# Performance work log

Measured on AMD Instinct MI355X. Metric: run time of the kernel, lower is better.

## Reference

```python
import jax, jax.numpy as jnp
import numpy as np

BLKQ = 64
BLKK = 64
TOPK_RATIO = 0.25
EPS = 1e-05


def mean_pool(x, blk):
    B, H, L, D = x.shape
    return x.reshape(B, H, L // blk, blk, D).mean(axis=3)


def setup_inputs() -> dict:
    key = jax.random.key(0)
    kq, kk, kv, kw, kb = jax.random.split(key, 5)
    B, H, Lq, Lk, D = 1, 8, 4096, 4096, 64
    q = jax.random.normal(kq, (B, H, Lq, D), dtype=jnp.float32)
    k = jax.random.normal(kk, (B, H, Lk, D), dtype=jnp.float32)
    v = jax.random.normal(kv, (B, H, Lk, D), dtype=jnp.float32)
    # proj_l is zero-initialized in the original; use small random weights so the
    # linear-attention branch contributes non-trivially to the output.
    proj_w = jax.random.normal(kw, (D, D), dtype=jnp.float32) * 0.02
    proj_b = jax.random.normal(kb, (D,), dtype=jnp.float32) * 0.02
    return {"q": q, "k": k, "v": v, "proj_w": proj_w, "proj_b": proj_b}


def reference(q, k, v, proj_w, proj_b):
    B, H, Lq, D = q.shape
    Lk = k.shape[2]
    nQ, nK = Lq // BLKQ, Lk // BLKK

    # ---- block-level top-k routing (get_block_map_cross) ----
    arg_k = k - k.mean(axis=-2, keepdims=True)
    pq = mean_pool(q, BLKQ)                      # (B,H,nQ,D)
    pk = mean_pool(arg_k, BLKK)                  # (B,H,nK,D)
    pooled_score = jnp.einsum('bhqd,bhkd->bhqk', pq, pk)  # (B,H,nQ,nK)
    topk = min(nK, max(1, int(TOPK_RATIO * nK)))
    lut = jax.lax.top_k(pooled_score, topk)[1]   # (B,H,nQ,topk) int32

    # ---- block-sparse cross attention (softmax over selected K blocks) ----
    qb = q.reshape(B, H, nQ, BLKQ, D)
    kb = k.reshape(B, H, nK, BLKK, D)
    vb = v.reshape(B, H, nK, BLKK, D)
    gather = jax.vmap(jax.vmap(lambda blocks, idx: blocks[idx]))  # over B,H
    kg = gather(kb, lut)                         # (B,H,nQ,topk,BLKK,D)
    vg = gather(vb, lut)                         # (B,H,nQ,topk,BLKK,D)
    scale = D ** -0.5
    s = jnp.einsum('bhnqd,bhntkd->bhnqtk', qb, kg) * scale
    s = s.reshape(B, H, nQ, BLKQ, topk * BLKK)
    p = jax.nn.softmax(s, axis=-1)
    o_s = jnp.einsum('bhnqt,bhntd->bhnqd', p, vg.reshape(B, H, nQ, topk * BLKK, D))
    o_s = o_s.reshape(B, H, Lq, D)

    # ---- linear attention branch (softmax feature map, tied q/k) ----
    qf = jax.nn.softmax(q, axis=-1)
    kf = jax.nn.softmax(k, axis=-1)
    kv = jnp.einsum('bhkd,bhke->bhde', kf, v)    # (B,H,D,D)
    denom = jnp.einsum('bhqd,bhd->bhq', qf, kf.sum(axis=2)) + EPS
    o_l = jnp.einsum('bhqd,bhde->bhqe', qf, kv) / denom[..., None]
    o_l = o_l @ proj_w.T + proj_b                # proj_l

    return o_s + o_l
```

## Files before the change

kernel.cpp:

```cpp
#include <hip/hip_runtime.h>
#include <math.h>

#define H 8
#define L 4096
#define D 64
#define NBLK 64
#define TOPK 16
#define EPS 1e-5f
#define LP 68

typedef unsigned short u16;
typedef unsigned int u32;
typedef __attribute__((ext_vector_type(8))) short bf16x8;
typedef __attribute__((ext_vector_type(16))) float f32x16;
typedef __attribute__((ext_vector_type(4))) u32 u32x4;

static __device__ __forceinline__ u16 f2bf(float x) {
  u32 u = __float_as_uint(x);
  u32 r = (u + 0x7fffu + ((u >> 16) & 1u)) >> 16;
  return (u16)r;
}
static __device__ __forceinline__ float bf2f(u16 h) {
  return __uint_as_float(((u32)h) << 16);
}
__device__ __forceinline__ float dot4f(float4 a, float4 b) {
  return a.x * b.x + a.y * b.y + a.z * b.z + a.w * b.w;
}
static __device__ __forceinline__ void async_cp16(uint4* lds, const uint4* g) {
  __builtin_amdgcn_global_load_lds(
      (const __attribute__((address_space(1))) void*)g,
      (__attribute__((address_space(3))) void*)lds, 16, 0, 0);
}

__global__ __launch_bounds__(256) void kvprep_kernel(
    const float* __restrict__ k, const float* __restrict__ v,
    u16* __restrict__ kpkb, u16* __restrict__ vpkb,
    float* __restrict__ pkp, float* __restrict__ part_kv,
    float* __restrict__ part_ks) {
  const int kb = blockIdx.x, h = blockIdx.y;
  __shared__ float kst[64 * LP];
  __shared__ float vst[64 * LP];
  __shared__ float red[4][64];
  const int t = threadIdx.x;

  {
    const float4* ksrc = (const float4*)(k + ((size_t)h * L + (size_t)kb * 64) * D);
    const float4* vsrc = (const float4*)(v + ((size_t)h * L + (size_t)kb * 64) * D);
#pragma unroll
    for (int i = 0; i < 4; ++i) {
      int flat = i * 256 + t;
      int row = flat >> 4, c4 = flat & 15;
      *(float4*)&kst[row * LP + c4 * 4] = ksrc[flat];
      *(float4*)&vst[row * LP + c4 * 4] = vsrc[flat];
    }
  }
  __syncthreads();

  {
    u16* rowbase = kpkb + ((size_t)h * L + (size_t)kb * 64) * 128;
#pragma unroll
    for (int pass = 0; pass < 2; ++pass) {
      const int key = pass * 32 + (t >> 3);
      const int sub = t & 7;
      float f[8];
#pragma unroll
      for (int e = 0; e < 8; ++e) f[e] = kst[key * LP + sub * 8 + e];
      u16 hi[8], lo[8];
#pragma unroll
      for (int e = 0; e < 8; ++e) {
        hi[e] = f2bf(f[e]);
        lo[e] = f2bf(f[e] - bf2f(hi[e]));
      }
      const int c = sub >> 1, g2 = sub & 1;
      u16* row = rowbase + (size_t)key * 128;
      const int sh = ((c * 4 + g2 * 2 + 0) ^ (key & 15)) * 8;
      const int sl = ((c * 4 + g2 * 2 + 1) ^ (key & 15)) * 8;
      uint4 vh = {(u32)hi[0] | ((u32)hi[1] << 16), (u32)hi[2] | ((u32)hi[3] << 16),
                  (u32)hi[4] | ((u32)hi[5] << 16), (u32)hi[6] | ((u32)hi[7] << 16)};
      uint4 vl = {(u32)lo[0] | ((u32)lo[1] << 16), (u32)lo[2] | ((u32)lo[3] << 16),
                  (u32)lo[4] | ((u32)lo[5] << 16), (u32)lo[6] | ((u32)lo[7] << 16)};
      *(uint4*)(row + sh) = vh;
      *(uint4*)(row + sl) = vl;
    }
  }

  {
    const int d = t & 63, rr = t >> 6;
    float s = 0.f;
#pragma unroll
    for (int i = 0; i < 16; ++i) s += kst[(rr * 16 + i) * LP + d];
    red[rr][d] = s;
  }
  __syncthreads();
  {
    const int d = t & 63, rr = t >> 6;
    if (rr == 0) {
      float tot = red[0][d] + red[1][d] + red[2][d] + red[3][d];
      pkp[((size_t)h * NBLK + kb) * D + d] = tot * (1.f / 64.f);
    }
  }

  {
    u16* base = vpkb + (((size_t)h * 64 + kb) * 64) * 128;
#pragma unroll
    for (int iter = 0; iter < 4; ++iter) {
      const int dim = iter * 16 + (t >> 4);
      const int s = t & 15;
      const int cgh = s ^ (dim & 15);
      const int c = cgh >> 2, g = (cgh >> 1) & 1, hl = cgh & 1;
      u16 o[8];
#pragma unroll
      for (int e = 0; e < 8; ++e) {
        const int key = 4 * g + (e & 3) + 8 * ((e >> 2) + 2 * (c & 1)) + 32 * (c >> 1);
        float val = vst[key * LP + dim];
        u16 hi = f2bf(val);
        o[e] = hl ? f2bf(val - bf2f(hi)) : hi;
      }
      uint4 pk4 = {(u32)o[0] | ((u32)o[1] << 16), (u32)o[2] | ((u32)o[3] << 16),
                   (u32)o[4] | ((u32)o[5] << 16), (u32)o[6] | ((u32)o[7] << 16)};
      *(uint4*)(base + (size_t)dim * 128 + s * 8) = pk4;
    }
  }

  if (t < 128) {
    const int row = t >> 1, half = t & 1;
    float4 kr[8];
#pragma unroll
    for (int i = 0; i < 8; ++i) kr[i] = *(float4*)&kst[row * LP + half * 32 + i * 4];
    float mxk = -INFINITY;
#pragma unroll
    for (int i = 0; i < 8; ++i)
      mxk = fmaxf(mxk, fmaxf(fmaxf(kr[i].x, kr[i].y), fmaxf(kr[i].z, kr[i].w)));
    mxk = fmaxf(mxk, __shfl_xor(mxk, 1));
    float smk = 0.f;
#pragma unroll
    for (int i = 0; i < 8; ++i) {
      kr[i].x = __expf(kr[i].x - mxk); kr[i].y = __expf(kr[i].y - mxk);
      kr[i].z = __expf(kr[i].z - mxk); kr[i].w = __expf(kr[i].w - mxk);
      smk += kr[i].x + kr[i].y + kr[i].z + kr[i].w;
    }
    smk += __shfl_xor(smk, 1);
    const float inv = 1.f / smk;
#pragma unroll
    for (int i = 0; i < 8; ++i) {
      float4 o = kr[i];
      o.x *= inv; o.y *= inv; o.z *= inv; o.w *= inv;
      *(float4*)&kst[row * LP + half * 32 + i * 4] = o;
    }
  }
  __syncthreads();

  {
    const int d = t & 63, eg = t >> 6;
    float4 acc0 = make_float4(0.f, 0.f, 0.f, 0.f);
    float4 acc1 = acc0, acc2 = acc0, acc3 = acc0;
    float ksacc = 0.f;
#pragma unroll 4
    for (int lr = 0; lr < 64; ++lr) {
      const float wv = kst[lr * LP + d];
      if (eg == 0) ksacc += wv;
      const float4* vr = (const float4*)&vst[lr * LP + eg * 16];
      float4 v0 = vr[0], v1 = vr[1], v2 = vr[2], v3 = vr[3];
      acc0.x += wv * v0.x; acc0.y += wv * v0.y; acc0.z += wv * v0.z; acc0.w += wv * v0.w;
      acc1.x += wv * v1.x; acc1.y += wv * v1.y; acc1.z += wv * v1.z; acc1.w += wv * v1.w;
      acc2.x += wv * v2.x; acc2.y += wv * v2.y; acc2.z += wv * v2.z; acc2.w += wv * v2.w;
      acc3.x += wv * v3.x; acc3.y += wv * v3.y; acc3.z += wv * v3.z; acc3.w += wv * v3.w;
    }
    float* kvb = part_kv + ((size_t)(h * 64 + kb)) * 4096 + (size_t)d * 64 + eg * 16;
    *(float4*)(kvb + 0) = acc0;
    *(float4*)(kvb + 4) = acc1;
    *(float4*)(kvb + 8) = acc2;
    *(float4*)(kvb + 12) = acc3;
    if (eg == 0) part_ks[(size_t)(h * 64 + kb) * 64 + d] = ksacc;
  }
}

__global__ __launch_bounds__(256) void pool_kernel(
    const float* __restrict__ src, float* __restrict__ dst) {
  const int blk = blockIdx.x, h = blockIdx.y;
  const int d = threadIdx.x & 63, rr = threadIdx.x >> 6;
  const float* base = src + ((size_t)h * L + (size_t)blk * 64) * D;
  float s = 0.f;
#pragma unroll
  for (int i = 0; i < 16; ++i) s += base[(rr * 16 + i) * D + d];
  __shared__ float red[4][64];
  red[rr][d] = s;
  __syncthreads();
  if (rr == 0) {
    float tot = red[0][d] + red[1][d] + red[2][d] + red[3][d];
    dst[((size_t)h * NBLK + blk) * D + d] = tot * (1.f / 64.f);
  }
}

__global__ __launch_bounds__(64) void topk_kernel(
    const float* __restrict__ pq, const float* __restrict__ pk,
    int* __restrict__ lut) {
  const int qb = blockIdx.x, h = blockIdx.y;
  const int j = threadIdx.x;
  const float4* pqv = (const float4*)(pq + ((size_t)h * NBLK + qb) * D);
  const float4* pkv = (const float4*)(pk + ((size_t)h * NBLK + j) * D);
  float s = 0.f;
#pragma unroll
  for (int d4 = 0; d4 < 16; ++d4) s += dot4f(pqv[d4], pkv[d4]);
  int* lrow = lut + ((size_t)h * NBLK + qb) * TOPK;
  for (int t = 0; t < TOPK; ++t) {
    float m = s;
    int mi = j;
#pragma unroll
    for (int off = 32; off; off >>= 1) {
      float om = __shfl_xor(m, off);
      int omi = __shfl_xor(mi, off);
      if (om > m || (om == m && omi < mi)) { m = om; mi = omi; }
    }
    if (j == 0) lrow[t] = mi;
    if (j == mi) s = -INFINITY;
  }
}

__global__ __launch_bounds__(256, 2) void sattn_kernel(
    const float* __restrict__ q, const u16* __restrict__ kpk,
    const u16* __restrict__ vpk, const int* __restrict__ lut,
    float* __restrict__ out) {
  __shared__ alignas(16) char smem[65536];
  const int bx = blockIdx.x;
  const int h = bx & 7, qb = bx >> 3;
  const int t = threadIdx.x;
  const int lane = t & 63;
  const int ln = lane & 31;
  const int g = lane >> 5;
  const int w = t >> 6;
  const int p = w & 1;
  const int kh = w >> 1;

  bf16x8 qh[4], ql[4];
  {
    const float* qrowp = q + ((size_t)h * L + (size_t)qb * 64 + p * 32 + ln) * D;
#pragma unroll
    for (int c = 0; c < 4; ++c) {
      float4 a = *(const float4*)(qrowp + c * 16 + g * 8);
      float4 b = *(const float4*)(qrowp + c * 16 + g * 8 + 4);
      float f[8] = {a.x, a.y, a.z, a.w, b.x, b.y, b.z, b.w};
#pragma unroll
      for (int e = 0; e < 8; ++e) {
        float x = f[e] * 0.125f;
        u16 hi = f2bf(x);
        qh[c][e] = (short)hi;
        ql[c][e] = (short)f2bf(x - bf2f(hi));
      }
    }
  }

  u16* bufA = (u16*)smem;
  u16* bufB = (u16*)smem + 16384;

  f32x16 o0, o1;
#pragma unroll
  for (int r = 0; r < 16; ++r) { o0[r] = 0.f; o1[r] = 0.f; }
  float lrun = 0.f;
  const int* lrow = lut + ((size_t)h * NBLK + qb) * TOPK;
  const int xr = ln & 15;
  const int krow = kh * 32 + ln;

#define STAGE(dst, kbi)                                                        \
  {                                                                            \
    const int kb_ = (kbi);                                                     \
    const uint4* gk = (const uint4*)(kpk + ((size_t)h * L + (size_t)kb_ * 64) * 128); \
    const uint4* gv = (const uint4*)(vpk + (((size_t)h * 64 + kb_) * 64) * 128);      \
    uint4* lk = (uint4*)(dst);                                                 \
    uint4* lv = (uint4*)((dst) + 8192);                                        \
    _Pragma("unroll") for (int i_ = 0; i_ < 4; ++i_) {                         \
      int x_ = i_ * 256 + t;                                                   \
      async_cp16(lk + x_, gk + x_);                                            \
      async_cp16(lv + x_, gv + x_);                                            \
    }                                                                          \
  }

  STAGE(bufA, lrow[0]);
  __syncthreads();

  u16* cur = bufA;
  u16* nxt = bufB;
  for (int ib = 0; ib < TOPK; ++ib) {
    if (ib + 1 < TOPK) STAGE(nxt, lrow[ib + 1]);

    const u16* KB = cur;
    const u16* VB = cur + 8192;

    f32x16 s0;
#pragma unroll
    for (int r = 0; r < 16; ++r) s0[r] = 0.f;
    __builtin_amdgcn_s_setprio(1);
#pragma unroll
    for (int c = 0; c < 4; ++c) {
      const int sH = c * 4 + g * 2;
      bf16x8 k_h = *(const bf16x8*)(KB + (size_t)krow * 128 + ((sH ^ xr) * 8));
      bf16x8 k_l = *(const bf16x8*)(KB + (size_t)krow * 128 + (((sH + 1) ^ xr) * 8));
      s0 = __builtin_amdgcn_mfma_f32_32x32x16_bf16(k_h, qh[c], s0, 0, 0, 0);
      s0 = __builtin_amdgcn_mfma_f32_32x32x16_bf16(k_l, qh[c], s0, 0, 0, 0);
      s0 = __builtin_amdgcn_mfma_f32_32x32x16_bf16(k_h, ql[c], s0, 0, 0, 0);
    }
    __builtin_amdgcn_s_setprio(0);

    u32 hpk[8], lpk[8];
    float psum = 0.f;
#pragma unroll
    for (int j = 0; j < 8; ++j) {
      float a = __expf(s0[2 * j]);
      float b = __expf(s0[2 * j + 1]);
      psum += a + b;
      u32 hp;
      asm("v_cvt_pk_bf16_f32 %0, %1, %2" : "=v"(hp) : "v"(a), "v"(b));
      hpk[j] = hp;
      float ah = __uint_as_float(hp << 16);
      float bh = __uint_as_float(hp & 0xffff0000u);
      u32 lp;
      asm("v_cvt_pk_bf16_f32 %0, %1, %2" : "=v"(lp) : "v"(a - ah), "v"(b - bh));
      lpk[j] = lp;
    }
    psum += __shfl_xor(psum, 32);
    lrun += psum;

    __builtin_amdgcn_s_setprio(1);
#pragma unroll
    for (int cc = 0; cc < 2; ++cc) {
      union { u32x4 u; bf16x8 b; } ph, pl;
      ph.u = (u32x4){hpk[4 * cc + 0], hpk[4 * cc + 1], hpk[4 * cc + 2], hpk[4 * cc + 3]};
      pl.u = (u32x4){lpk[4 * cc + 0], lpk[4 * cc + 1], lpk[4 * cc + 2], lpk[4 * cc + 3]};
      const bf16x8 pah = ph.b, pal = pl.b;
      const int sH = (2 * kh + cc) * 4 + g * 2;
      bf16x8 v0h = *(const bf16x8*)(VB + (size_t)ln * 128 + ((sH ^ xr) * 8));
      bf16x8 v0l = *(const bf16x8*)(VB + (size_t)ln * 128 + (((sH + 1) ^ xr) * 8));
      bf16x8 v1h = *(const bf16x8*)(VB + (size_t)(32 + ln) * 128 + ((sH ^ xr) * 8));
      bf16x8 v1l = *(const bf16x8*)(VB + (size_t)(32 + ln) * 128 + (((sH + 1) ^ xr) * 8));
      o0 = __builtin_amdgcn_mfma_f32_32x32x16_bf16(pah, v0h, o0, 0, 0, 0);
      o0 = __builtin_amdgcn_mfma_f32_32x32x16_bf16(pal, v0h, o0, 0, 0, 0);
      o0 = __builtin_amdgcn_mfma_f32_32x32x16_bf16(pah, v0l, o0, 0, 0, 0);
      o1 = __builtin_amdgcn_mfma_f32_32x32x16_bf16(pah, v1h, o1, 0, 0, 0);
      o1 = __builtin_amdgcn_mfma_f32_32x32x16_bf16(pal, v1h, o1, 0, 0, 0);
      o1 = __builtin_amdgcn_mfma_f32_32x32x16_bf16(pah, v1l, o1, 0, 0, 0);
    }
    __builtin_amdgcn_s_setprio(0);

    __syncthreads();
    u16* tmp = cur; cur = nxt; nxt = tmp;
  }
#undef STAGE

  float* oxbase = (float*)smem;
  float* lxbase = (float*)smem + 4096;
  if (g == 0) lxbase[(p * 2 + kh) * 32 + ln] = lrun;
  if (kh == 1) {
#pragma unroll
    for (int r = 0; r < 16; ++r) {
      const int R = (r & 3) + 8 * (r >> 2) + 4 * g;
      oxbase[p * 2048 + R * 64 + ln] = o0[r];
      oxbase[p * 2048 + R * 64 + 32 + ln] = o1[r];
    }
  }
  __syncthreads();
  if (kh == 0) {
#pragma unroll
    for (int r = 0; r < 16; ++r) {
      const int R = (r & 3) + 8 * (r >> 2) + 4 * g;
      const float lt = lxbase[(p * 2 + 0) * 32 + R] + lxbase[(p * 2 + 1) * 32 + R];
      const float inv = 1.f / lt;
      const size_t row = (size_t)h * L + (size_t)qb * 64 + p * 32 + R;
      out[row * 64 + ln] = (o0[r] + oxbase[p * 2048 + R * 64 + ln]) * inv;
      out[row * 64 + 32 + ln] = (o1[r] + oxbase[p * 2048 + R * 64 + 32 + ln]) * inv;
    }
  }
}

__global__ __launch_bounds__(256) void kvred_kernel(
    const float* __restrict__ part_kv, const float* __restrict__ part_ks,
    float* __restrict__ p2kv, float* __restrict__ p2ks) {
  const int j = blockIdx.x, h = blockIdx.y;
  const int t = threadIdx.x;
  float4 s0 = make_float4(0.f, 0.f, 0.f, 0.f);
  float4 s1 = s0, s2 = s0, s3 = s0;
#pragma unroll
  for (int p = 0; p < 4; ++p) {
    const float4* src = (const float4*)(part_kv + ((size_t)(h * 64 + j * 4 + p)) * 4096);
    float4 a = src[0 * 256 + t], b = src[1 * 256 + t];
    float4 c = src[2 * 256 + t], d = src[3 * 256 + t];
    s0.x += a.x; s0.y += a.y; s0.z += a.z; s0.w += a.w;
    s1.x += b.x; s1.y += b.y; s1.z += b.z; s1.w += b.w;
    s2.x += c.x; s2.y += c.y; s2.z += c.z; s2.w += c.w;
    s3.x += d.x; s3.y += d.y; s3.z += d.z; s3.w += d.w;
  }
  float4* dst = (float4*)(p2kv + ((size_t)(h * 16 + j)) * 4096);
  dst[0 * 256 + t] = s0;
  dst[1 * 256 + t] = s1;
  dst[2 * 256 + t] = s2;
  dst[3 * 256 + t] = s3;
  if (t < 64) {
    float ks = 0.f;
#pragma unroll
    for (int p = 0; p < 4; ++p) ks += part_ks[(size_t)(h * 64 + j * 4 + p) * 64 + t];
    p2ks[(size_t)(h * 16 + j) * 64 + t] = ks;
  }
}

__global__ __launch_bounds__(256) void kvproj_kernel(
    const float* __restrict__ p2kv, const float* __restrict__ p2ks,
    const float* __restrict__ pw, float* __restrict__ kvp,
    float* __restrict__ ksum) {
  const int h = blockIdx.x;
  __shared__ float kvs[64 * 64];
  __shared__ float pws[64 * 64];
  const int t = threadIdx.x;
  float4 s0 = make_float4(0.f, 0.f, 0.f, 0.f);
  float4 s1 = s0, s2 = s0, s3 = s0;
  for (int p = 0; p < 16; ++p) {
    const float4* src = (const float4*)(p2kv + ((size_t)(h * 16 + p)) * 4096);
    float4 a = src[0 * 256 + t], b = src[1 * 256 + t];
    float4 cc = src[2 * 256 + t], dd = src[3 * 256 + t];
    s0.x += a.x; s0.y += a.y; s0.z += a.z; s0.w += a.w;
    s1.x += b.x; s1.y += b.y; s1.z += b.z; s1.w += b.w;
    s2.x += cc.x; s2.y += cc.y; s2.z += cc.z; s2.w += cc.w;
    s3.x += dd.x; s3.y += dd.y; s3.z += dd.z; s3.w += dd.w;
  }
  ((float4*)kvs)[0 * 256 + t] = s0;
  ((float4*)kvs)[1 * 256 + t] = s1;
  ((float4*)kvs)[2 * 256 + t] = s2;
  ((float4*)kvs)[3 * 256 + t] = s3;
#pragma unroll
  for (int i = 0; i < 4; ++i) {
    int f4 = i * 256 + t;
    ((float4*)pws)[f4] = ((const float4*)pw)[f4];
  }
  if (t < 64) {
    float ks = 0.f;
    for (int p = 0; p < 16; ++p) ks += p2ks[(size_t)(h * 16 + p) * 64 + t];
    ksum[(size_t)h * 64 + t] = ks;
  }
  __syncthreads();
  const int d = t & 63, fg = t >> 6;
  float* dst = kvp + (size_t)h * 4096 + (size_t)d * 64;
  const float4* a = (const float4*)&kvs[d * 64];
  for (int f = fg * 16; f < fg * 16 + 16; ++f) {
    const float4* b = (const float4*)&pws[f * 64];
    float s = 0.f;
#pragma unroll
    for (int e4 = 0; e4 < 16; ++e4) s += dot4f(a[e4], b[e4]);
    dst[f] = s;
  }
}

__global__ __launch_bounds__(256) void linattn_kernel(
    const float* __restrict__ q, const float* __restrict__ kvp,
    const float* __restrict__ ksum, const float* __restrict__ pb,
    float* __restrict__ out) {
  __shared__ float kvs[64 * 64];
  __shared__ float kss[64], pbs[64];
  const int t = threadIdx.x;
  const size_t grow = (size_t)blockIdx.x * 256 + t;
  const int h = (int)(grow >> 12);
#pragma unroll
  for (int i = 0; i < 4; ++i) {
    int f4 = i * 256 + t;
    ((float4*)kvs)[f4] = ((const float4*)(kvp + (size_t)h * 4096))[f4];
  }
  if (t < 64) {
    kss[t] = ksum[(size_t)h * 64 + t];
    pbs[t] = pb[t];
  }
  __syncthreads();
  const float* qrow = q + grow * 64;
  float mx = -INFINITY;
  const float4* q4p = (const float4*)qrow;
#pragma unroll
  for (int i = 0; i < 16; ++i) {
    float4 x = q4p[i];
    mx = fmaxf(mx, fmaxf(fmaxf(x.x, x.y), fmaxf(x.z, x.w)));
  }
  float4 tt[16];
#pragma unroll
  for (int i = 0; i < 16; ++i) tt[i] = make_float4(0.f, 0.f, 0.f, 0.f);
  float sm = 0.f, dn = 0.f;
#pragma unroll 4
  for (int dd = 0; dd < 64; ++dd) {
    const float wv = __expf(qrow[dd] - mx);
    sm += wv;
    dn += wv * kss[dd];
    const float4* kvr = (const float4*)&kvs[dd * 64];
#pragma unroll
    for (int e4 = 0; e4 < 16; ++e4) {
      float4 kk = kvr[e4];
      tt[e4].x += wv * kk.x; tt[e4].y += wv * kk.y;
      tt[e4].z += wv * kk.z; tt[e4].w += wv * kk.w;
    }
  }
  const float inv = 1.f / (dn + EPS * sm);
  float* orow = out + grow * 64;
#pragma unroll
  for (int e4 = 0; e4 < 16; ++e4) {
    float4 o = ((float4*)orow)[e4];
    o.x += tt[e4].x * inv + pbs[e4 * 4 + 0];
    o.y += tt[e4].y * inv + pbs[e4 * 4 + 1];
    o.z += tt[e4].z * inv + pbs[e4 * 4 + 2];
    o.w += tt[e4].w * inv + pbs[e4 * 4 + 3];
    ((float4*)orow)[e4] = o;
  }
}

extern "C" void kernel_launch(void* const* d_in, const int* in_sizes, int n_in,
                              void* d_out, int out_size, void* d_ws, size_t ws_size,
                              hipStream_t stream) {
  const float* q = (const float*)d_in[0];
  const float* k = (const float*)d_in[1];
  const float* v = (const float*)d_in[2];
  const float* pw = (const float*)d_in[3];
  const float* pb = (const float*)d_in[4];
  float* out = (float*)d_out;

  u16* kpkb = (u16*)d_ws;
  u16* vpkb = (u16*)d_ws + 4194304;
  float* fws = (float*)((char*)d_ws + 16777216);
  float* pq = fws;
  float* pk = fws + 32768;
  float* part_kv = fws + 65536;
  float* part_ks = fws + 2162688;
  float* p2kv = fws + 2195456;
  float* p2ks = fws + 2719744;
  float* kvp = fws + 2727936;
  float* ksum = fws + 2760704;
  int* lut = (int*)(fws + 2761216);

  kvprep_kernel<<<dim3(64, 8), 256, 0, stream>>>(k, v, kpkb, vpkb, pk, part_kv, part_ks);
  pool_kernel<<<dim3(64, 8), 256, 0, stream>>>(q, pq);
  topk_kernel<<<dim3(64, 8), 64, 0, stream>>>(pq, pk, lut);
  sattn_kernel<<<512, 256, 0, stream>>>(q, kpkb, vpkb, lut, out);
  kvred_kernel<<<dim3(16, 8), 256, 0, stream>>>(part_kv, part_ks, p2kv, p2ks);
  kvproj_kernel<<<8, 256, 0, stream>>>(p2kv, p2ks, pw, kvp, ksum);
  linattn_kernel<<<128, 256, 0, stream>>>(q, kvp, ksum, pb, out);
}
```

Measured before the change: 172.0 us.

## Split sparse attention over two halves of top-k blocks, merge in linattn

Splits each query block's 16 selected key blocks into two halves handled by separate workgroups, doubling the grid. Each half writes unnormalized partial outputs and row sums, and the linear-attention kernel combines them. LDS drops to a single buffer with register prefetch instead of async global-to-LDS double buffering, which allows 4 blocks per CU. The cost is extra partial-output traffic, an extra sync per iteration, and merging without a max subtraction, which relies on the scores not being shifted by a running max.

```diff
diff --git a/kernel.cpp b/kernel.cpp
--- a/kernel.cpp
+++ b/kernel.cpp
@@ -25,11 +25,6 @@
 }
 __device__ __forceinline__ float dot4f(float4 a, float4 b) {
   return a.x * b.x + a.y * b.y + a.z * b.z + a.w * b.w;
-}
-static __device__ __forceinline__ void async_cp16(uint4* lds, const uint4* g) {
-  __builtin_amdgcn_global_load_lds(
-      (const __attribute__((address_space(1))) void*)g,
-      (__attribute__((address_space(3))) void*)lds, 16, 0, 0);
 }
 
 __global__ __launch_bounds__(256) void kvprep_kernel(
@@ -217,13 +212,15 @@
   }
 }
 
-__global__ __launch_bounds__(256, 2) void sattn_kernel(
+__global__ __launch_bounds__(256, 4) void sattn_kernel(
     const float* __restrict__ q, const u16* __restrict__ kpk,
     const u16* __restrict__ vpk, const int* __restrict__ lut,
-    float* __restrict__ out) {
-  __shared__ alignas(16) char smem[65536];
+    float* __restrict__ part_o, float* __restrict__ part_l) {
+  __shared__ alignas(16) char smem[32768];
   const int bx = blockIdx.x;
-  const int h = bx & 7, qb = bx >> 3;
+  const int h = bx & 7;
+  const int qb = (bx >> 3) & 63;
+  const int hs = bx >> 9;
   const int t = threadIdx.x;
   const int lane = t & 63;
   const int ln = lane & 31;
@@ -250,42 +247,40 @@
     }
   }
 
-  u16* bufA = (u16*)smem;
-  u16* bufB = (u16*)smem + 16384;
+  uint4* lk = (uint4*)smem;
+  uint4* lv = lk + 1024;
+  const u16* KB = (const u16*)smem;
+  const u16* VB = (const u16*)smem + 8192;
 
   f32x16 o0, o1;
 #pragma unroll
   for (int r = 0; r < 16; ++r) { o0[r] = 0.f; o1[r] = 0.f; }
   float lrun = 0.f;
-  const int* lrow = lut + ((size_t)h * NBLK + qb) * TOPK;
+  const int* lrow = lut + ((size_t)h * NBLK + qb) * TOPK + hs * 8;
   const int xr = ln & 15;
   const int krow = kh * 32 + ln;
 
-#define STAGE(dst, kbi)                                                        \
-  {                                                                            \
-    const int kb_ = (kbi);                                                     \
+  uint4 pf[8];
+#define LOADR(kbi)                                                               \
+  {                                                                              \
+    const int kb_ = (kbi);                                                       \
     const uint4* gk = (const uint4*)(kpk + ((size_t)h * L + (size_t)kb_ * 64) * 128); \
     const uint4* gv = (const uint4*)(vpk + (((size_t)h * 64 + kb_) * 64) * 128);      \
-    uint4* lk = (uint4*)(dst);                                                 \
-    uint4* lv = (uint4*)((dst) + 8192);                                        \
-    _Pragma("unroll") for (int i_ = 0; i_ < 4; ++i_) {                         \
-      int x_ = i_ * 256 + t;                                                   \
-      async_cp16(lk + x_, gk + x_);                                            \
-      async_cp16(lv + x_, gv + x_);                                            \
-    }                                                                          \
-  }
-
-  STAGE(bufA, lrow[0]);
-  __syncthreads();
-
-  u16* cur = bufA;
-  u16* nxt = bufB;
-  for (int ib = 0; ib < TOPK; ++ib) {
-    if (ib + 1 < TOPK) STAGE(nxt, lrow[ib + 1]);
-
-    const u16* KB = cur;
-    const u16* VB = cur + 8192;
-
+    _Pragma("unroll") for (int i_ = 0; i_ < 4; ++i_) pf[i_] = gk[i_ * 256 + t];  \
+    _Pragma("unroll") for (int i_ = 0; i_ < 4; ++i_) pf[4 + i_] = gv[i_ * 256 + t]; \
+  }
+#define WRITES                                                                   \
+  {                                                                              \
+    _Pragma("unroll") for (int i_ = 0; i_ < 4; ++i_) lk[i_ * 256 + t] = pf[i_];  \
+    _Pragma("unroll") for (int i_ = 0; i_ < 4; ++i_) lv[i_ * 256 + t] = pf[4 + i_]; \
+  }
+
+  LOADR(lrow[0]);
+  WRITES;
+  LOADR(lrow[1]);
+  __syncthreads();
+
+  for (int ib = 0; ib < 8; ++ib) {
     f32x16 s0;
 #pragma unroll
     for (int r = 0; r < 16; ++r) s0[r] = 0.f;
@@ -342,9 +337,12 @@
     __builtin_amdgcn_s_setprio(0);
 
     __syncthreads();
-    u16* tmp = cur; cur = nxt; nxt = tmp;
-  }
-#undef STAGE
+    if (ib + 1 < 8) { WRITES; }
+    if (ib + 2 < 8) LOADR(lrow[ib + 2]);
+    __syncthreads();
+  }
+#undef LOADR
+#undef WRITES
 
   float* oxbase = (float*)smem;
   float* lxbase = (float*)smem + 4096;
@@ -359,14 +357,15 @@
   }
   __syncthreads();
   if (kh == 0) {
+    const size_t rbase = (size_t)hs * (H * L) + (size_t)h * L + (size_t)qb * 64 + p * 32;
 #pragma unroll
     for (int r = 0; r < 16; ++r) {
       const int R = (r & 3) + 8 * (r >> 2) + 4 * g;
       const float lt = lxbase[(p * 2 + 0) * 32 + R] + lxbase[(p * 2 + 1) * 32 + R];
-      const float inv = 1.f / lt;
-      const size_t row = (size_t)h * L + (size_t)qb * 64 + p * 32 + R;
-      out[row * 64 + ln] = (o0[r] + oxbase[p * 2048 + R * 64 + ln]) * inv;
-      out[row * 64 + 32 + ln] = (o1[r] + oxbase[p * 2048 + R * 64 + 32 + ln]) * inv;
+      if (ln == 0) part_l[rbase + R] = lt;
+      const size_t row = rbase + R;
+      part_o[row * 64 + ln] = o0[r] + oxbase[p * 2048 + R * 64 + ln];
+      part_o[row * 64 + 32 + ln] = o1[r] + oxbase[p * 2048 + R * 64 + 32 + ln];
     }
   }
 }
@@ -450,6 +449,7 @@
 __global__ __launch_bounds__(256) void linattn_kernel(
     const float* __restrict__ q, const float* __restrict__ kvp,
     const float* __restrict__ ksum, const float* __restrict__ pb,
+    const float* __restrict__ part_o, const float* __restrict__ part_l,
     float* __restrict__ out) {
   __shared__ float kvs[64 * 64];
   __shared__ float kss[64], pbs[64];
@@ -492,14 +492,18 @@
     }
   }
   const float inv = 1.f / (dn + EPS * sm);
+  const float sinv = 1.f / (part_l[grow] + part_l[(size_t)H * L + grow]);
+  const float4* po0 = (const float4*)(part_o + grow * 64);
+  const float4* po1 = (const float4*)(part_o + ((size_t)H * L + grow) * 64);
   float* orow = out + grow * 64;
 #pragma unroll
   for (int e4 = 0; e4 < 16; ++e4) {
-    float4 o = ((float4*)orow)[e4];
-    o.x += tt[e4].x * inv + pbs[e4 * 4 + 0];
-    o.y += tt[e4].y * inv + pbs[e4 * 4 + 1];
-    o.z += tt[e4].z * inv + pbs[e4 * 4 + 2];
-    o.w += tt[e4].w * inv + pbs[e4 * 4 + 3];
+    float4 a = po0[e4], b = po1[e4];
+    float4 o;
+    o.x = (a.x + b.x) * sinv + tt[e4].x * inv + pbs[e4 * 4 + 0];
+    o.y = (a.y + b.y) * sinv + tt[e4].y * inv + pbs[e4 * 4 + 1];
+    o.z = (a.z + b.z) * sinv + tt[e4].z * inv + pbs[e4 * 4 + 2];
+    o.w = (a.w + b.w) * sinv + tt[e4].w * inv + pbs[e4 * 4 + 3];
     ((float4*)orow)[e4] = o;
   }
 }
@@ -526,12 +530,14 @@
   float* kvp = fws + 2727936;
   float* ksum = fws + 2760704;
   int* lut = (int*)(fws + 2761216);
+  float* part_l = fws + 2769408;
+  float* part_o = fws + 2834944;
 
   kvprep_kernel<<<dim3(64, 8), 256, 0, stream>>>(k, v, kpkb, vpkb, pk, part_kv, part_ks);
   pool_kernel<<<dim3(64, 8), 256, 0, stream>>>(q, pq);
   topk_kernel<<<dim3(64, 8), 64, 0, stream>>>(pq, pk, lut);
-  sattn_kernel<<<512, 256, 0, stream>>>(q, kpkb, vpkb, lut, out);
+  sattn_kernel<<<1024, 256, 0, stream>>>(q, kpkb, vpkb, lut, part_o, part_l);
   kvred_kernel<<<dim3(16, 8), 256, 0, stream>>>(part_kv, part_ks, p2kv, p2ks);
   kvproj_kernel<<<8, 256, 0, stream>>>(p2kv, p2ks, pw, kvp, ksum);
-  linattn_kernel<<<128, 256, 0, stream>>>(q, kvp, ksum, pb, out);
-}
+  linattn_kernel<<<128, 256, 0, stream>>>(q, kvp, ksum, pb, part_o, part_l, out);
+}
```

After: 255.7 us. 1.49x slower.
